# Performance work log

Measured on AMD Instinct MI355X. Metric: run time of the kernel, lower is better.

The kernel has to match this reference:

```python
import jax, jax.numpy as jnp
import numpy as np

EPS = 1e-12  # torch F.normalize clamp_min eps


def _agnn_conv(x, src, dst, beta, n):
    # x: [N, D]; src/dst: [E] (message flows src -> dst, softmax over dst's in-edges)
    xn = x / jnp.maximum(jnp.linalg.norm(x, axis=-1, keepdims=True), EPS)
    alpha = beta[0] * jnp.sum(xn[src] * xn[dst], axis=-1)            # [E] cosine sim * beta
    amax = jax.ops.segment_max(alpha, dst, num_segments=n)           # stable segment softmax
    ex = jnp.exp(alpha - amax[dst])
    denom = jax.ops.segment_sum(ex, dst, num_segments=n)
    w = ex / denom[dst]                                              # [E]
    return jax.ops.segment_sum(x[src] * w[:, None], dst, num_segments=n)


def setup_inputs() -> dict:
    key = jax.random.key(0)
    ks = jax.random.split(key, 8)
    N, E, G = 131072, 4194304, 2048
    x = jax.random.normal(ks[0], (N, 75), dtype=jnp.float32)
    edge_index = jax.random.randint(ks[1], (2, E), 0, N, dtype=jnp.int64)
    batch = jnp.sort(jax.random.randint(ks[2], (N,), 0, G, dtype=jnp.int64))
    lin1_w = jax.random.normal(ks[3], (16, 75), dtype=jnp.float32) * (1.0 / np.sqrt(75))
    lin1_b = jnp.zeros((16,), jnp.float32)
    beta1 = jnp.ones((1,), jnp.float32)   # prop1: requires_grad=False, beta=1
    beta2 = jnp.ones((1,), jnp.float32)   # prop2: learnable beta, init 1
    lin2_w = jax.random.normal(ks[4], (64, 16), dtype=jnp.float32) * (1.0 / np.sqrt(16))
    lin2_b = jnp.zeros((64,), jnp.float32)
    gather_w = jax.random.normal(ks[5], (1, 64), dtype=jnp.float32) * (1.0 / np.sqrt(64))
    gather_b = jnp.zeros((1,), jnp.float32)
    return {"x": x, "edge_index": edge_index, "batch": batch, "num_graphs": G,
            "lin1_w": lin1_w, "lin1_b": lin1_b, "beta1": beta1, "beta2": beta2,
            "lin2_w": lin2_w, "lin2_b": lin2_b, "gather_w": gather_w, "gather_b": gather_b}


def reference(x, edge_index, batch, num_graphs, lin1_w, lin1_b, beta1, beta2,
              lin2_w, lin2_b, gather_w, gather_b):
    n = x.shape[0]
    # PyG AGNNConv adds self-loops by default
    loops = jnp.arange(n, dtype=edge_index.dtype)
    src = jnp.concatenate([edge_index[0], loops])
    dst = jnp.concatenate([edge_index[1], loops])
    # dropout is identity in eval mode
    h = jax.nn.relu(x @ lin1_w.T + lin1_b)          # [N, 16]
    h = _agnn_conv(h, src, dst, beta1, n)
    h = _agnn_conv(h, src, dst, beta2, n)
    h = h @ lin2_w.T + lin2_b                        # [N, 64]
    y = jax.ops.segment_sum(h, batch, num_segments=num_graphs)  # global_add_pool [G, 64]
    return y @ gather_w.T + gather_b                 # [G, 1]
```

## Files before the change

kernel.cpp:

```cpp
#include <hip/hip_runtime.h>
#include <hip/hip_bf16.h>
#include <hip/hip_fp16.h>
#include <math.h>

#define SSEPS 1e-24f
#define NPB 256
#define NPB_SHIFT 8
#define SRC_BITS 17
#define SRC_MASK ((1 << SRC_BITS) - 1)
#define NB 512
#define CAP_B 8832
#define SC_EDGES 4096
#define SCB 512
#define MG_T 512
#define MG_LIN 4096
#define CSR_T 512

union QRowU2 { int4 v; _Float16 h[8]; };


__global__ __launch_bounds__(MG_T) void mega1(
    const int* __restrict__ src, const int* __restrict__ dst, int E,
    int* __restrict__ gcnt, int* __restrict__ packed, int nScat,
    const float* __restrict__ x, const float* __restrict__ W1,
    const float* __restrict__ b1, int* __restrict__ rec1, int N, int D,
    const float* __restrict__ l2w, const float* __restrict__ l2b,
    const float* __restrict__ gw, float* __restrict__ vbuf,
    float* __restrict__ out, const float* __restrict__ gb, int G) {
    __shared__ int sh[1216];
    int bid = blockIdx.x;
    int t = threadIdx.x;

    if (bid < nScat) {
        int* h = sh;
        int* dl = sh + SCB;
        int base = bid * SC_EDGES;
        int ed[8], es[8];
        int nv = 0;
#pragma unroll
        for (int k = 0; k < 8; ++k) {
            int i = base + k * MG_T + t;
            if (i < E) {
                ed[nv] = __builtin_nontemporal_load(&dst[i]);
                es[nv] = __builtin_nontemporal_load(&src[i]);
                ++nv;
            }
        }
        h[t] = 0;
        __syncthreads();
        for (int k = 0; k < nv; ++k) atomicAdd(&h[ed[k] >> NPB_SHIFT], 1);
        __syncthreads();
        {
            int c = h[t];
            int gp = c ? atomicAdd(&gcnt[t], c) : 0;
            dl[t] = t * CAP_B + gp;
            h[t] = 0;
        }
        __syncthreads();
        for (int k = 0; k < nv; ++k) {
            int d = ed[k];
            int b = d >> NPB_SHIFT;
            int pos = atomicAdd(&h[b], 1);
            int gi = dl[b] + pos;
            if (gi < (b + 1) * CAP_B)
                packed[gi] = ((d & (NPB - 1)) << SRC_BITS) | es[k];
        }
    } else if (bid < nScat + MG_LIN) {
        float* Ws = (float*)sh;
        float* Bs = (float*)sh + 1200;
        for (int i = t; i < 16 * D; i += MG_T) Ws[i] = W1[i];
        if (t < 16) Bs[t] = b1[t];
        __syncthreads();
        int node = (bid - nScat) * (MG_T >> 4) + (t >> 4);
        int c = t & 15;
        if (node >= N) return;
        const float* xr = x + (size_t)node * D;
        float acc = Bs[c];
        for (int k = 0; k < D; ++k) acc = fmaf(xr[k], Ws[c * D + k], acc);
        float hv = fmaxf(acc, 0.f);
        float hn = __shfl_xor(hv, 1);
        if (!(c & 1)) {
            union { _Float16 hh[2]; int i; } u;
            u.hh[0] = (_Float16)hv;
            u.hh[1] = (_Float16)hn;
            rec1[8 * node + (c >> 1)] = u.i;
        }
    } else if (bid == nScat + MG_LIN) {
        if (t < 16) {
            float a = 0.f;
            for (int j = 0; j < 64; ++j) a = fmaf(gw[j], l2w[j * 16 + t], a);
            vbuf[t] = a;
        } else if (t == 16) {
            float a = 0.f;
            for (int j = 0; j < 64; ++j) a = fmaf(gw[j], l2b[j], a);
            vbuf[16] = a;
        }
    } else {
        int g = (bid - (nScat + MG_LIN + 1)) * MG_T + t;
        if (g < G) out[g] = gb[0];
    }
}

__global__ __launch_bounds__(CSR_T) void csr_build(
    const int* __restrict__ packed, const int* __restrict__ gcnt,
    int* __restrict__ deg, int* __restrict__ offs,
    int* __restrict__ csr_src, int N) {
    __shared__ int ldeg[NPB];
    __shared__ int lcur[NPB];
    __shared__ int wsum[4];
    int b = blockIdx.x;
    int t = threadIdx.x;
    int e0 = b * CAP_B;
    int cnt = gcnt[b];
    if (cnt > CAP_B) cnt = CAP_B;
    if (t < NPB) ldeg[t] = 0;
    __syncthreads();
    for (int i = t; i < cnt; i += CSR_T)
        atomicAdd(&ldeg[packed[e0 + i] >> SRC_BITS], 1);
    __syncthreads();
    if (t < NPB) {
        int v = ldeg[t];
        int lane = t & 63;
        int incl = v;
#pragma unroll
        for (int off = 1; off < 64; off <<= 1) {
            int up = __shfl_up(incl, off);
            if (lane >= off) incl += up;
        }
        if (lane == 63) wsum[t >> 6] = incl;
        lcur[t] = incl - v;
    }
    __syncthreads();
    if (t < NPB) {
        int w = t >> 6;
        int basep = 0;
        for (int k = 0; k < w; ++k) basep += wsum[k];
        int ex = lcur[t] + basep;
        int node = (b << NPB_SHIFT) + t;
        if (node < N) {
            deg[node] = ldeg[t];
            offs[node] = e0 + ex;
        }
        lcur[t] = ex;
    }
    __syncthreads();
    for (int i = t; i < cnt; i += CSR_T) {
        int p = packed[e0 + i];
        int pos = atomicAdd(&lcur[p >> SRC_BITS], 1);
        csr_src[e0 + pos] = p & SRC_MASK;
    }
}

__global__ __launch_bounds__(256) void agnn_conv1(
    const int* __restrict__ rec1,
    const int* __restrict__ offs, const int* __restrict__ deg,
    const int* __restrict__ csr, const float* __restrict__ beta_p,
    int* __restrict__ rec2, int N) {
    int tid = blockIdx.x * blockDim.x + threadIdx.x;
    int node = tid >> 1;
    int q = tid & 1;
    if (node >= N) return;
    float beta = beta_p[0];
    const int4* rp = (const int4*)rec1;

    QRowU2 rdu;
    rdu.v = rp[2 * node + q];
    float xd[8];
#pragma unroll
    for (int k = 0; k < 8; ++k) xd[k] = (float)rdu.h[k];

    float ssd = 0.f;
#pragma unroll
    for (int k = 0; k < 8; ++k) ssd = fmaf(xd[k], xd[k], ssd);
    ssd += __shfl_xor(ssd, 1);
    float invsd = rsqrtf(fmaxf(ssd, SSEPS));

    float e0 = __expf(beta * ssd * invsd * invsd);
    float denom = e0;
    float acc[8];
#pragma unroll
    for (int k = 0; k < 8; ++k) acc[k] = e0 * xd[k];

    int start = offs[node], cnt = deg[node];
    int i = 0;
    for (; i + 8 <= cnt; i += 8) {
        int j[8];
        QRowU2 r[8];
#pragma unroll
        for (int u = 0; u < 8; ++u) j[u] = __builtin_nontemporal_load(&csr[start + i + u]);
#pragma unroll
        for (int u = 0; u < 8; ++u) r[u].v = rp[2 * j[u] + q];
#pragma unroll
        for (int u = 0; u < 8; ++u) {
            float d = 0.f, ss = 0.f;
            float hs[8];
#pragma unroll
            for (int k = 0; k < 8; ++k) {
                hs[k] = (float)r[u].h[k];
                d = fmaf(xd[k], hs[k], d);
                ss = fmaf(hs[k], hs[k], ss);
            }
            d += __shfl_xor(d, 1);
            ss += __shfl_xor(ss, 1);
            float ee = __expf(beta * d * invsd * rsqrtf(fmaxf(ss, SSEPS)));
            denom += ee;
#pragma unroll
            for (int k = 0; k < 8; ++k) acc[k] = fmaf(ee, hs[k], acc[k]);
        }
    }
    for (; i < cnt; ++i) {
        int j = __builtin_nontemporal_load(&csr[start + i]);
        QRowU2 r;
        r.v = rp[2 * j + q];
        float d = 0.f, ss = 0.f;
        float hs[8];
#pragma unroll
        for (int k = 0; k < 8; ++k) {
            hs[k] = (float)r.h[k];
            d = fmaf(xd[k], hs[k], d);
            ss = fmaf(hs[k], hs[k], ss);
        }
        d += __shfl_xor(d, 1);
        ss += __shfl_xor(ss, 1);
        float ee = __expf(beta * d * invsd * rsqrtf(fmaxf(ss, SSEPS)));
        denom += ee;
#pragma unroll
        for (int k = 0; k < 8; ++k) acc[k] = fmaf(ee, hs[k], acc[k]);
    }

    float inv = 1.f / denom;
    QRowU2 w;
#pragma unroll
    for (int k = 0; k < 8; ++k) w.h[k] = (_Float16)(acc[k] * inv);
    ((int4*)rec2)[2 * node + q] = w.v;
}

__global__ __launch_bounds__(256) void agnn_conv2(
    const int* __restrict__ rec2,
    const int* __restrict__ offs, const int* __restrict__ deg,
    const int* __restrict__ csr, const float* __restrict__ beta_p,
    const float* __restrict__ vbuf, const int* __restrict__ batch,
    float* __restrict__ out, int N) {
    int tid = blockIdx.x * blockDim.x + threadIdx.x;
    int node = tid >> 1;
    int q = tid & 1;
    if (node >= N) return;
    float beta = beta_p[0];
    const int4* rp = (const int4*)rec2;

    float vq[8];
#pragma unroll
    for (int k = 0; k < 8; ++k) vq[k] = vbuf[8 * q + k];

    QRowU2 rdu;
    rdu.v = rp[2 * node + q];
    float xd[8];
#pragma unroll
    for (int k = 0; k < 8; ++k) xd[k] = (float)rdu.h[k];

    float ssd = 0.f, pd = 0.f;
#pragma unroll
    for (int k = 0; k < 8; ++k) {
        ssd = fmaf(xd[k], xd[k], ssd);
        pd = fmaf(vq[k], xd[k], pd);
    }
    ssd += __shfl_xor(ssd, 1);
    pd += __shfl_xor(pd, 1);
    float invsd = rsqrtf(fmaxf(ssd, SSEPS));

    float e0 = __expf(beta * ssd * invsd * invsd);
    float denom = e0;
    float acc = e0 * pd;

    int start = offs[node], cnt = deg[node];
    int i = 0;
    for (; i + 8 <= cnt; i += 8) {
        int j[8];
        QRowU2 r[8];
#pragma unroll
        for (int u = 0; u < 8; ++u) j[u] = __builtin_nontemporal_load(&csr[start + i + u]);
#pragma unroll
        for (int u = 0; u < 8; ++u) r[u].v = rp[2 * j[u] + q];
#pragma unroll
        for (int u = 0; u < 8; ++u) {
            float d = 0.f, ss = 0.f, pv = 0.f;
#pragma unroll
            for (int k = 0; k < 8; ++k) {
                float hs = (float)r[u].h[k];
                d = fmaf(xd[k], hs, d);
                ss = fmaf(hs, hs, ss);
                pv = fmaf(vq[k], hs, pv);
            }
            d += __shfl_xor(d, 1);
            ss += __shfl_xor(ss, 1);
            pv += __shfl_xor(pv, 1);
            float ee = __expf(beta * d * invsd * rsqrtf(fmaxf(ss, SSEPS)));
            denom += ee;
            acc = fmaf(ee, pv, acc);
        }
    }
    for (; i < cnt; ++i) {
        int j = __builtin_nontemporal_load(&csr[start + i]);
        QRowU2 r;
        r.v = rp[2 * j + q];
        float d = 0.f, ss = 0.f, pv = 0.f;
#pragma unroll
        for (int k = 0; k < 8; ++k) {
            float hs = (float)r.h[k];
            d = fmaf(xd[k], hs, d);
            ss = fmaf(hs, hs, ss);
            pv = fmaf(vq[k], hs, pv);
        }
        d += __shfl_xor(d, 1);
        ss += __shfl_xor(ss, 1);
        pv += __shfl_xor(pv, 1);
        float ee = __expf(beta * d * invsd * rsqrtf(fmaxf(ss, SSEPS)));
        denom += ee;
        acc = fmaf(ee, pv, acc);
    }
    if (q == 0) atomicAdd(&out[batch[node]], acc / denom + vbuf[16]);
}


extern "C" void kernel_launch(void* const* d_in, const int* in_sizes, int n_in,
                              void* d_out, int out_size, void* d_ws, size_t ws_size,
                              hipStream_t stream) {
    const float* x = (const float*)d_in[0];
    const int* edge_index = (const int*)d_in[1];
    const int* batch = (const int*)d_in[2];
    const float* lin1_w = (const float*)d_in[4];
    const float* lin1_b = (const float*)d_in[5];
    const float* beta1 = (const float*)d_in[6];
    const float* beta2 = (const float*)d_in[7];
    const float* lin2_w = (const float*)d_in[8];
    const float* lin2_b = (const float*)d_in[9];
    const float* gather_w = (const float*)d_in[10];
    const float* gather_b = (const float*)d_in[11];
    float* out = (float*)d_out;

    const int N = in_sizes[2];
    const int E = in_sizes[1] / 2;
    const int D = in_sizes[0] / N;
    const int G = out_size;

    const int* src = edge_index;
    const int* dst = edge_index + E;

    float* w = (float*)d_ws;
    int* rec1 = (int*)w;                 w += (size_t)N * 8;
    int* rec2 = (int*)w;                 w += (size_t)N * 8;
    float* vbuf = w;                     w += 32;
    int* deg = (int*)w;                  w += N;
    int* offs = (int*)w;                 w += N;
    int* packed = (int*)w;               w += (size_t)NB * CAP_B;
    int* csr_src = (int*)w;              w += (size_t)NB * CAP_B;
    int* gcnt = (int*)w;                 w += NB;

    const int B = 256;
    dim3 gridNode2((2 * N + B - 1) / B);

    hipMemsetAsync(gcnt, 0, NB * sizeof(int), stream);

    int nScat = (E + SC_EDGES - 1) / SC_EDGES;
    int nLin = (N + (MG_T / 16) - 1) / (MG_T / 16);
    int nOut = (G + MG_T - 1) / MG_T;
    dim3 megaGrid(nScat + nLin + 1 + nOut);
    mega1<<<megaGrid, MG_T, 0, stream>>>(src, dst, E, gcnt, packed, nScat,
                                         x, lin1_w, lin1_b, rec1, N, D,
                                         lin2_w, lin2_b, gather_w, vbuf,
                                         out, gather_b, G);

    csr_build<<<dim3(NB), CSR_T, 0, stream>>>(packed, gcnt, deg, offs,
                                              csr_src, N);

    agnn_conv1<<<gridNode2, B, 0, stream>>>(rec1, offs, deg, csr_src,
                                            beta1, rec2, N);
    agnn_conv2<<<gridNode2, B, 0, stream>>>(rec2, offs, deg, csr_src,
                                            beta2, vbuf, batch, out, N);
}
```

Measured before the change: 332.7 us.

## Sort nodes by degree and split each row across four lanes

Adds a degree histogram in csr_build, plus a scan and a counting-sort scatter that build a degree-ordered permutation of nodes with their offsets and degrees. Both AGNN convolution kernels now walk nodes in that order, so each wavefront handles nodes of similar degree and loses less time to divergent loop trip counts. Each node row is also split across four lanes loading 8 bytes each instead of two lanes loading 16 bytes, with an extra shuffle stage per reduction. This costs two extra small kernel launches and an indirection through perm, and neighbouring nodes in a wave are no longer contiguous when their rows are read and written.

```diff
diff --git a/kernel.cpp b/kernel.cpp
--- a/kernel.cpp
+++ b/kernel.cpp
@@ -15,8 +15,9 @@
 #define MG_T 512
 #define MG_LIN 4096
 #define CSR_T 512
-
-union QRowU2 { int4 v; _Float16 h[8]; };
+#define DBINS 256
+
+union QRowU { int2 v; _Float16 h[4]; };
 
 
 __global__ __launch_bounds__(MG_T) void mega1(
@@ -104,9 +105,10 @@
 __global__ __launch_bounds__(CSR_T) void csr_build(
     const int* __restrict__ packed, const int* __restrict__ gcnt,
     int* __restrict__ deg, int* __restrict__ offs,
-    int* __restrict__ csr_src, int N) {
+    int* __restrict__ csr_src, int* __restrict__ hist, int N) {
     __shared__ int ldeg[NPB];
     __shared__ int lcur[NPB];
+    __shared__ int lhist[DBINS];
     __shared__ int wsum[4];
     int b = blockIdx.x;
     int t = threadIdx.x;
@@ -114,12 +116,14 @@
     int cnt = gcnt[b];
     if (cnt > CAP_B) cnt = CAP_B;
     if (t < NPB) ldeg[t] = 0;
+    if (t < DBINS) lhist[t] = 0;
     __syncthreads();
     for (int i = t; i < cnt; i += CSR_T)
         atomicAdd(&ldeg[packed[e0 + i] >> SRC_BITS], 1);
     __syncthreads();
     if (t < NPB) {
         int v = ldeg[t];
+        atomicAdd(&lhist[v < DBINS ? v : DBINS - 1], 1);
         int lane = t & 63;
         int incl = v;
 #pragma unroll
@@ -143,157 +147,214 @@
         }
         lcur[t] = ex;
     }
+    if (t < DBINS && t >= NPB) {}
     __syncthreads();
     for (int i = t; i < cnt; i += CSR_T) {
         int p = packed[e0 + i];
         int pos = atomicAdd(&lcur[p >> SRC_BITS], 1);
         csr_src[e0 + pos] = p & SRC_MASK;
     }
+    if (t < DBINS && lhist[t]) atomicAdd(&hist[t], lhist[t]);
+}
+
+__global__ void deg_scan(const int* __restrict__ hist, int* __restrict__ cursor) {
+    __shared__ int s[DBINS];
+    int t = threadIdx.x;
+    int h = hist[t];
+    s[t] = h;
+    __syncthreads();
+    for (int off = 1; off < DBINS; off <<= 1) {
+        int a = (t >= off) ? s[t - off] : 0;
+        __syncthreads();
+        s[t] += a;
+        __syncthreads();
+    }
+    cursor[t] = s[t] - h;
+}
+
+__global__ void deg_scatter(const int* __restrict__ deg, const int* __restrict__ offs,
+                            int* __restrict__ cursor, int* __restrict__ perm,
+                            int* __restrict__ sdeg, int* __restrict__ soffs, int N) {
+    __shared__ int lh[DBINS];
+    __shared__ int lb[DBINS];
+    int t = threadIdx.x;
+    if (t < DBINS) lh[t] = 0;
+    __syncthreads();
+    int i = blockIdx.x * blockDim.x + t;
+    int bin = 0, r = 0, dv = 0;
+    if (i < N) {
+        dv = deg[i];
+        bin = dv < DBINS ? dv : DBINS - 1;
+        r = atomicAdd(&lh[bin], 1);
+    }
+    __syncthreads();
+    if (t < DBINS && lh[t]) lb[t] = atomicAdd(&cursor[t], lh[t]);
+    __syncthreads();
+    if (i < N) {
+        int p = lb[bin] + r;
+        perm[p] = i;
+        sdeg[p] = dv;
+        soffs[p] = offs[i];
+    }
 }
 
 __global__ __launch_bounds__(256) void agnn_conv1(
     const int* __restrict__ rec1,
-    const int* __restrict__ offs, const int* __restrict__ deg,
-    const int* __restrict__ csr, const float* __restrict__ beta_p,
+    const int* __restrict__ soffs, const int* __restrict__ sdeg,
+    const int* __restrict__ csr, const int* __restrict__ perm,
+    const float* __restrict__ beta_p,
     int* __restrict__ rec2, int N) {
     int tid = blockIdx.x * blockDim.x + threadIdx.x;
-    int node = tid >> 1;
-    int q = tid & 1;
-    if (node >= N) return;
+    int slot = tid >> 2;
+    int q = tid & 3;
+    if (slot >= N) return;
+    int node = perm[slot];
     float beta = beta_p[0];
-    const int4* rp = (const int4*)rec1;
-
-    QRowU2 rdu;
-    rdu.v = rp[2 * node + q];
-    float xd[8];
-#pragma unroll
-    for (int k = 0; k < 8; ++k) xd[k] = (float)rdu.h[k];
+    const int2* rp = (const int2*)rec1;
+
+    QRowU rdu;
+    rdu.v = rp[4 * node + q];
+    float xd[4];
+#pragma unroll
+    for (int k = 0; k < 4; ++k) xd[k] = (float)rdu.h[k];
 
     float ssd = 0.f;
 #pragma unroll
-    for (int k = 0; k < 8; ++k) ssd = fmaf(xd[k], xd[k], ssd);
+    for (int k = 0; k < 4; ++k) ssd = fmaf(xd[k], xd[k], ssd);
     ssd += __shfl_xor(ssd, 1);
+    ssd += __shfl_xor(ssd, 2);
     float invsd = rsqrtf(fmaxf(ssd, SSEPS));
 
     float e0 = __expf(beta * ssd * invsd * invsd);
     float denom = e0;
-    float acc[8];
-#pragma unroll
-    for (int k = 0; k < 8; ++k) acc[k] = e0 * xd[k];
-
-    int start = offs[node], cnt = deg[node];
+    float acc[4];
+#pragma unroll
+    for (int k = 0; k < 4; ++k) acc[k] = e0 * xd[k];
+
+    int start = soffs[slot], cnt = sdeg[slot];
     int i = 0;
     for (; i + 8 <= cnt; i += 8) {
         int j[8];
-        QRowU2 r[8];
+        QRowU r[8];
 #pragma unroll
         for (int u = 0; u < 8; ++u) j[u] = __builtin_nontemporal_load(&csr[start + i + u]);
 #pragma unroll
-        for (int u = 0; u < 8; ++u) r[u].v = rp[2 * j[u] + q];
+        for (int u = 0; u < 8; ++u) r[u].v = rp[4 * j[u] + q];
 #pragma unroll
         for (int u = 0; u < 8; ++u) {
             float d = 0.f, ss = 0.f;
-            float hs[8];
-#pragma unroll
-            for (int k = 0; k < 8; ++k) {
+            float hs[4];
+#pragma unroll
+            for (int k = 0; k < 4; ++k) {
                 hs[k] = (float)r[u].h[k];
                 d = fmaf(xd[k], hs[k], d);
                 ss = fmaf(hs[k], hs[k], ss);
             }
             d += __shfl_xor(d, 1);
+            d += __shfl_xor(d, 2);
             ss += __shfl_xor(ss, 1);
+            ss += __shfl_xor(ss, 2);
             float ee = __expf(beta * d * invsd * rsqrtf(fmaxf(ss, SSEPS)));
             denom += ee;
 #pragma unroll
-            for (int k = 0; k < 8; ++k) acc[k] = fmaf(ee, hs[k], acc[k]);
+            for (int k = 0; k < 4; ++k) acc[k] = fmaf(ee, hs[k], acc[k]);
         }
     }
     for (; i < cnt; ++i) {
         int j = __builtin_nontemporal_load(&csr[start + i]);
-        QRowU2 r;
-        r.v = rp[2 * j + q];
+        QRowU r;
+        r.v = rp[4 * j + q];
         float d = 0.f, ss = 0.f;
-        float hs[8];
-#pragma unroll
-        for (int k = 0; k < 8; ++k) {
+        float hs[4];
+#pragma unroll
+        for (int k = 0; k < 4; ++k) {
             hs[k] = (float)r.h[k];
             d = fmaf(xd[k], hs[k], d);
             ss = fmaf(hs[k], hs[k], ss);
         }
         d += __shfl_xor(d, 1);
+        d += __shfl_xor(d, 2);
         ss += __shfl_xor(ss, 1);
+        ss += __shfl_xor(ss, 2);
         float ee = __expf(beta * d * invsd * rsqrtf(fmaxf(ss, SSEPS)));
         denom += ee;
 #pragma unroll
-        for (int k = 0; k < 8; ++k) acc[k] = fmaf(ee, hs[k], acc[k]);
+        for (int k = 0; k < 4; ++k) acc[k] = fmaf(ee, hs[k], acc[k]);
     }
 
     float inv = 1.f / denom;
-    QRowU2 w;
-#pragma unroll
-    for (int k = 0; k < 8; ++k) w.h[k] = (_Float16)(acc[k] * inv);
-    ((int4*)rec2)[2 * node + q] = w.v;
+    QRowU w;
+#pragma unroll
+    for (int k = 0; k < 4; ++k) w.h[k] = (_Float16)(acc[k] * inv);
+    ((int2*)rec2)[4 * node + q] = w.v;
 }
 
 __global__ __launch_bounds__(256) void agnn_conv2(
     const int* __restrict__ rec2,
-    const int* __restrict__ offs, const int* __restrict__ deg,
-    const int* __restrict__ csr, const float* __restrict__ beta_p,
+    const int* __restrict__ soffs, const int* __restrict__ sdeg,
+    const int* __restrict__ csr, const int* __restrict__ perm,
+    const float* __restrict__ beta_p,
     const float* __restrict__ vbuf, const int* __restrict__ batch,
     float* __restrict__ out, int N) {
     int tid = blockIdx.x * blockDim.x + threadIdx.x;
-    int node = tid >> 1;
-    int q = tid & 1;
-    if (node >= N) return;
+    int slot = tid >> 2;
+    int q = tid & 3;
+    if (slot >= N) return;
+    int node = perm[slot];
     float beta = beta_p[0];
-    const int4* rp = (const int4*)rec2;
-
-    float vq[8];
-#pragma unroll
-    for (int k = 0; k < 8; ++k) vq[k] = vbuf[8 * q + k];
-
-    QRowU2 rdu;
-    rdu.v = rp[2 * node + q];
-    float xd[8];
-#pragma unroll
-    for (int k = 0; k < 8; ++k) xd[k] = (float)rdu.h[k];
+    const int2* rp = (const int2*)rec2;
+
+    float vq[4];
+#pragma unroll
+    for (int k = 0; k < 4; ++k) vq[k] = vbuf[4 * q + k];
+
+    QRowU rdu;
+    rdu.v = rp[4 * node + q];
+    float xd[4];
+#pragma unroll
+    for (int k = 0; k < 4; ++k) xd[k] = (float)rdu.h[k];
 
     float ssd = 0.f, pd = 0.f;
 #pragma unroll
-    for (int k = 0; k < 8; ++k) {
+    for (int k = 0; k < 4; ++k) {
         ssd = fmaf(xd[k], xd[k], ssd);
         pd = fmaf(vq[k], xd[k], pd);
     }
     ssd += __shfl_xor(ssd, 1);
+    ssd += __shfl_xor(ssd, 2);
     pd += __shfl_xor(pd, 1);
+    pd += __shfl_xor(pd, 2);
     float invsd = rsqrtf(fmaxf(ssd, SSEPS));
 
     float e0 = __expf(beta * ssd * invsd * invsd);
     float denom = e0;
     float acc = e0 * pd;
 
-    int start = offs[node], cnt = deg[node];
+    int start = soffs[slot], cnt = sdeg[slot];
     int i = 0;
     for (; i + 8 <= cnt; i += 8) {
         int j[8];
-        QRowU2 r[8];
+        QRowU r[8];
 #pragma unroll
         for (int u = 0; u < 8; ++u) j[u] = __builtin_nontemporal_load(&csr[start + i + u]);
 #pragma unroll
-        for (int u = 0; u < 8; ++u) r[u].v = rp[2 * j[u] + q];
+        for (int u = 0; u < 8; ++u) r[u].v = rp[4 * j[u] + q];
 #pragma unroll
         for (int u = 0; u < 8; ++u) {
             float d = 0.f, ss = 0.f, pv = 0.f;
 #pragma unroll
-            for (int k = 0; k < 8; ++k) {
+            for (int k = 0; k < 4; ++k) {
                 float hs = (float)r[u].h[k];
                 d = fmaf(xd[k], hs, d);
                 ss = fmaf(hs, hs, ss);
                 pv = fmaf(vq[k], hs, pv);
             }
             d += __shfl_xor(d, 1);
+            d += __shfl_xor(d, 2);
             ss += __shfl_xor(ss, 1);
+            ss += __shfl_xor(ss, 2);
             pv += __shfl_xor(pv, 1);
+            pv += __shfl_xor(pv, 2);
             float ee = __expf(beta * d * invsd * rsqrtf(fmaxf(ss, SSEPS)));
             denom += ee;
             acc = fmaf(ee, pv, acc);
@@ -301,19 +362,22 @@
     }
     for (; i < cnt; ++i) {
         int j = __builtin_nontemporal_load(&csr[start + i]);
-        QRowU2 r;
-        r.v = rp[2 * j + q];
+        QRowU r;
+        r.v = rp[4 * j + q];
         float d = 0.f, ss = 0.f, pv = 0.f;
 #pragma unroll
-        for (int k = 0; k < 8; ++k) {
+        for (int k = 0; k < 4; ++k) {
             float hs = (float)r.h[k];
             d = fmaf(xd[k], hs, d);
             ss = fmaf(hs, hs, ss);
             pv = fmaf(vq[k], hs, pv);
         }
         d += __shfl_xor(d, 1);
+        d += __shfl_xor(d, 2);
         ss += __shfl_xor(ss, 1);
+        ss += __shfl_xor(ss, 2);
         pv += __shfl_xor(pv, 1);
+        pv += __shfl_xor(pv, 2);
         float ee = __expf(beta * d * invsd * rsqrtf(fmaxf(ss, SSEPS)));
         denom += ee;
         acc = fmaf(ee, pv, acc);
@@ -355,11 +419,16 @@
     int* packed = (int*)w;               w += (size_t)NB * CAP_B;
     int* csr_src = (int*)w;              w += (size_t)NB * CAP_B;
     int* gcnt = (int*)w;                 w += NB;
+    int* hist = (int*)w;                 w += DBINS;
+    int* cursor = (int*)w;               w += DBINS;
+    int* perm = (int*)w;                 w += N;
+    int* sdeg = (int*)w;                 w += N;
+    int* soffs = (int*)w;                w += N;
 
     const int B = 256;
-    dim3 gridNode2((2 * N + B - 1) / B);
-
-    hipMemsetAsync(gcnt, 0, NB * sizeof(int), stream);
+    dim3 gridNode4((4 * N + B - 1) / B);
+
+    hipMemsetAsync(gcnt, 0, (NB + DBINS) * sizeof(int), stream);
 
     int nScat = (E + SC_EDGES - 1) / SC_EDGES;
     int nLin = (N + (MG_T / 16) - 1) / (MG_T / 16);
@@ -371,10 +440,14 @@
                                          out, gather_b, G);
 
     csr_build<<<dim3(NB), CSR_T, 0, stream>>>(packed, gcnt, deg, offs,
-                                              csr_src, N);
-
-    agnn_conv1<<<gridNode2, B, 0, stream>>>(rec1, offs, deg, csr_src,
+                                              csr_src, hist, N);
+
+    deg_scan<<<dim3(1), DBINS, 0, stream>>>(hist, cursor);
+    deg_scatter<<<dim3((N + B - 1) / B), B, 0, stream>>>(deg, offs, cursor, perm,
+                                                         sdeg, soffs, N);
+
+    agnn_conv1<<<gridNode4, B, 0, stream>>>(rec1, soffs, sdeg, csr_src, perm,
                                             beta1, rec2, N);
-    agnn_conv2<<<gridNode2, B, 0, stream>>>(rec2, offs, deg, csr_src,
+    agnn_conv2<<<gridNode4, B, 0, stream>>>(rec2, soffs, sdeg, csr_src, perm,
                                             beta2, vbuf, batch, out, N);
 }
```

Measured after the change: 329.8 us. About the same (-0.8%).

## Drop CSR build; aggregate edges per destination bucket with LDS atomics

Applied to the files above, without the earlier changes.

Removes the csr_build kernel along with the deg/offs/csr_src arrays. Each of 512 blocks of 1024 threads now walks its destination bucket of packed edges directly. Per-node accumulators live in shared memory and are updated with LDS float atomics, so no per-node sorted adjacency is needed. This saves a kernel launch and the CSR write/read traffic, but adds shared-memory atomic contention and uses only 512 blocks, which may limit occupancy. It also relies on the softmax max being skipped, which is safe because the cosine similarity is bounded.

```diff
diff --git a/kernel.cpp b/kernel.cpp
--- a/kernel.cpp
+++ b/kernel.cpp
@@ -14,9 +14,7 @@
 #define SCB 512
 #define MG_T 512
 #define MG_LIN 4096
-#define CSR_T 512
-
-union QRowU2 { int4 v; _Float16 h[8]; };
+#define CV_T 1024
 
 
 __global__ __launch_bounds__(MG_T) void mega1(
@@ -101,224 +99,175 @@
     }
 }
 
-__global__ __launch_bounds__(CSR_T) void csr_build(
-    const int* __restrict__ packed, const int* __restrict__ gcnt,
-    int* __restrict__ deg, int* __restrict__ offs,
-    int* __restrict__ csr_src, int N) {
-    __shared__ int ldeg[NPB];
-    __shared__ int lcur[NPB];
-    __shared__ int wsum[4];
+__global__ __launch_bounds__(CV_T) void conv1p(
+    const int* __restrict__ rec1, const int* __restrict__ packed,
+    const int* __restrict__ gcnt, const float* __restrict__ beta_p,
+    int* __restrict__ rec2, int N) {
+    __shared__ float xs[NPB * 17];
+    __shared__ float as[NPB * 17];
     int b = blockIdx.x;
     int t = threadIdx.x;
-    int e0 = b * CAP_B;
+    float beta = beta_p[0];
+
+    {
+        int ln = t >> 2;
+        int qq = t & 3;
+        int node = (b << NPB_SHIFT) + ln;
+        union { int2 v; _Float16 h[4]; } u;
+        u.v = ((const int2*)rec1)[4 * node + qq];
+        float f0 = (float)u.h[0], f1 = (float)u.h[1];
+        float f2 = (float)u.h[2], f3 = (float)u.h[3];
+        float ss = f0 * f0 + f1 * f1 + f2 * f2 + f3 * f3;
+        ss += __shfl_xor(ss, 1);
+        ss += __shfl_xor(ss, 2);
+        float invsd = rsqrtf(fmaxf(ss, SSEPS));
+        float e0 = __expf(beta * ss * invsd * invsd);
+        int base = ln * 17 + qq * 4;
+        xs[base + 0] = f0; xs[base + 1] = f1;
+        xs[base + 2] = f2; xs[base + 3] = f3;
+        as[base + 0] = e0 * f0; as[base + 1] = e0 * f1;
+        as[base + 2] = e0 * f2; as[base + 3] = e0 * f3;
+        if (qq == 0) {
+            xs[ln * 17 + 16] = invsd;
+            as[ln * 17 + 16] = e0;
+        }
+    }
+    __syncthreads();
+
     int cnt = gcnt[b];
     if (cnt > CAP_B) cnt = CAP_B;
-    if (t < NPB) ldeg[t] = 0;
+    const int* pk = packed + b * CAP_B;
+    const int4* rp = (const int4*)rec1;
+    for (int i = t; i < cnt; i += CV_T) {
+        int p = __builtin_nontemporal_load(&pk[i]);
+        int d = p >> SRC_BITS;
+        int s = p & SRC_MASK;
+        int4 r0 = rp[2 * s];
+        int4 r1 = rp[2 * s + 1];
+        int base = d * 17;
+        float invsd = xs[base + 16];
+        union { int4 v; _Float16 h[8]; } u0, u1;
+        u0.v = r0; u1.v = r1;
+        float dot = 0.f, ss = 0.f;
+#pragma unroll
+        for (int k = 0; k < 8; ++k) {
+            float f = (float)u0.h[k];
+            dot = fmaf(xs[base + k], f, dot);
+            ss = fmaf(f, f, ss);
+        }
+#pragma unroll
+        for (int k = 0; k < 8; ++k) {
+            float f = (float)u1.h[k];
+            dot = fmaf(xs[base + 8 + k], f, dot);
+            ss = fmaf(f, f, ss);
+        }
+        float ee = __expf(beta * dot * invsd * rsqrtf(fmaxf(ss, SSEPS)));
+#pragma unroll
+        for (int k = 0; k < 8; ++k)
+            atomicAdd(&as[base + k], ee * (float)u0.h[k]);
+#pragma unroll
+        for (int k = 0; k < 8; ++k)
+            atomicAdd(&as[base + 8 + k], ee * (float)u1.h[k]);
+        atomicAdd(&as[base + 16], ee);
+    }
     __syncthreads();
-    for (int i = t; i < cnt; i += CSR_T)
-        atomicAdd(&ldeg[packed[e0 + i] >> SRC_BITS], 1);
-    __syncthreads();
-    if (t < NPB) {
-        int v = ldeg[t];
-        int lane = t & 63;
-        int incl = v;
-#pragma unroll
-        for (int off = 1; off < 64; off <<= 1) {
-            int up = __shfl_up(incl, off);
-            if (lane >= off) incl += up;
-        }
-        if (lane == 63) wsum[t >> 6] = incl;
-        lcur[t] = incl - v;
-    }
-    __syncthreads();
-    if (t < NPB) {
-        int w = t >> 6;
-        int basep = 0;
-        for (int k = 0; k < w; ++k) basep += wsum[k];
-        int ex = lcur[t] + basep;
-        int node = (b << NPB_SHIFT) + t;
-        if (node < N) {
-            deg[node] = ldeg[t];
-            offs[node] = e0 + ex;
-        }
-        lcur[t] = ex;
-    }
-    __syncthreads();
-    for (int i = t; i < cnt; i += CSR_T) {
-        int p = packed[e0 + i];
-        int pos = atomicAdd(&lcur[p >> SRC_BITS], 1);
-        csr_src[e0 + pos] = p & SRC_MASK;
+
+    {
+        int ln = t >> 2;
+        int qq = t & 3;
+        int node = (b << NPB_SHIFT) + ln;
+        float inv = 1.f / as[ln * 17 + 16];
+        union { int2 v; _Float16 h[4]; } w;
+#pragma unroll
+        for (int k = 0; k < 4; ++k)
+            w.h[k] = (_Float16)(as[ln * 17 + qq * 4 + k] * inv);
+        if (node < N) ((int2*)rec2)[4 * node + qq] = w.v;
     }
 }
 
-__global__ __launch_bounds__(256) void agnn_conv1(
-    const int* __restrict__ rec1,
-    const int* __restrict__ offs, const int* __restrict__ deg,
-    const int* __restrict__ csr, const float* __restrict__ beta_p,
-    int* __restrict__ rec2, int N) {
-    int tid = blockIdx.x * blockDim.x + threadIdx.x;
-    int node = tid >> 1;
-    int q = tid & 1;
-    if (node >= N) return;
-    float beta = beta_p[0];
-    const int4* rp = (const int4*)rec1;
-
-    QRowU2 rdu;
-    rdu.v = rp[2 * node + q];
-    float xd[8];
-#pragma unroll
-    for (int k = 0; k < 8; ++k) xd[k] = (float)rdu.h[k];
-
-    float ssd = 0.f;
-#pragma unroll
-    for (int k = 0; k < 8; ++k) ssd = fmaf(xd[k], xd[k], ssd);
-    ssd += __shfl_xor(ssd, 1);
-    float invsd = rsqrtf(fmaxf(ssd, SSEPS));
-
-    float e0 = __expf(beta * ssd * invsd * invsd);
-    float denom = e0;
-    float acc[8];
-#pragma unroll
-    for (int k = 0; k < 8; ++k) acc[k] = e0 * xd[k];
-
-    int start = offs[node], cnt = deg[node];
-    int i = 0;
-    for (; i + 8 <= cnt; i += 8) {
-        int j[8];
-        QRowU2 r[8];
-#pragma unroll
-        for (int u = 0; u < 8; ++u) j[u] = __builtin_nontemporal_load(&csr[start + i + u]);
-#pragma unroll
-        for (int u = 0; u < 8; ++u) r[u].v = rp[2 * j[u] + q];
-#pragma unroll
-        for (int u = 0; u < 8; ++u) {
-            float d = 0.f, ss = 0.f;
-            float hs[8];
-#pragma unroll
-            for (int k = 0; k < 8; ++k) {
-                hs[k] = (float)r[u].h[k];
-                d = fmaf(xd[k], hs[k], d);
-                ss = fmaf(hs[k], hs[k], ss);
-            }
-            d += __shfl_xor(d, 1);
-            ss += __shfl_xor(ss, 1);
-            float ee = __expf(beta * d * invsd * rsqrtf(fmaxf(ss, SSEPS)));
-            denom += ee;
-#pragma unroll
-            for (int k = 0; k < 8; ++k) acc[k] = fmaf(ee, hs[k], acc[k]);
-        }
-    }
-    for (; i < cnt; ++i) {
-        int j = __builtin_nontemporal_load(&csr[start + i]);
-        QRowU2 r;
-        r.v = rp[2 * j + q];
-        float d = 0.f, ss = 0.f;
-        float hs[8];
-#pragma unroll
-        for (int k = 0; k < 8; ++k) {
-            hs[k] = (float)r.h[k];
-            d = fmaf(xd[k], hs[k], d);
-            ss = fmaf(hs[k], hs[k], ss);
-        }
-        d += __shfl_xor(d, 1);
-        ss += __shfl_xor(ss, 1);
-        float ee = __expf(beta * d * invsd * rsqrtf(fmaxf(ss, SSEPS)));
-        denom += ee;
-#pragma unroll
-        for (int k = 0; k < 8; ++k) acc[k] = fmaf(ee, hs[k], acc[k]);
-    }
-
-    float inv = 1.f / denom;
-    QRowU2 w;
-#pragma unroll
-    for (int k = 0; k < 8; ++k) w.h[k] = (_Float16)(acc[k] * inv);
-    ((int4*)rec2)[2 * node + q] = w.v;
-}
-
-__global__ __launch_bounds__(256) void agnn_conv2(
-    const int* __restrict__ rec2,
-    const int* __restrict__ offs, const int* __restrict__ deg,
-    const int* __restrict__ csr, const float* __restrict__ beta_p,
+__global__ __launch_bounds__(CV_T) void conv2p(
+    const int* __restrict__ rec2, const int* __restrict__ packed,
+    const int* __restrict__ gcnt, const float* __restrict__ beta_p,
     const float* __restrict__ vbuf, const int* __restrict__ batch,
     float* __restrict__ out, int N) {
-    int tid = blockIdx.x * blockDim.x + threadIdx.x;
-    int node = tid >> 1;
-    int q = tid & 1;
-    if (node >= N) return;
+    __shared__ float xs[NPB * 17];
+    __shared__ float as[NPB * 3];
+    int b = blockIdx.x;
+    int t = threadIdx.x;
     float beta = beta_p[0];
+    float v[16];
+#pragma unroll
+    for (int k = 0; k < 16; ++k) v[k] = vbuf[k];
+    float c0 = vbuf[16];
+
+    {
+        int ln = t >> 2;
+        int qq = t & 3;
+        int node = (b << NPB_SHIFT) + ln;
+        union { int2 v; _Float16 h[4]; } u;
+        u.v = ((const int2*)rec2)[4 * node + qq];
+        float f0 = (float)u.h[0], f1 = (float)u.h[1];
+        float f2 = (float)u.h[2], f3 = (float)u.h[3];
+        float ss = f0 * f0 + f1 * f1 + f2 * f2 + f3 * f3;
+        float pd = v[qq * 4 + 0] * f0 + v[qq * 4 + 1] * f1 +
+                   v[qq * 4 + 2] * f2 + v[qq * 4 + 3] * f3;
+        ss += __shfl_xor(ss, 1);
+        ss += __shfl_xor(ss, 2);
+        pd += __shfl_xor(pd, 1);
+        pd += __shfl_xor(pd, 2);
+        float invsd = rsqrtf(fmaxf(ss, SSEPS));
+        float e0 = __expf(beta * ss * invsd * invsd);
+        int base = ln * 17 + qq * 4;
+        xs[base + 0] = f0; xs[base + 1] = f1;
+        xs[base + 2] = f2; xs[base + 3] = f3;
+        if (qq == 0) {
+            xs[ln * 17 + 16] = invsd;
+            as[ln * 3 + 0] = e0 * pd;
+            as[ln * 3 + 1] = e0;
+        }
+    }
+    __syncthreads();
+
+    int cnt = gcnt[b];
+    if (cnt > CAP_B) cnt = CAP_B;
+    const int* pk = packed + b * CAP_B;
     const int4* rp = (const int4*)rec2;
-
-    float vq[8];
-#pragma unroll
-    for (int k = 0; k < 8; ++k) vq[k] = vbuf[8 * q + k];
-
-    QRowU2 rdu;
-    rdu.v = rp[2 * node + q];
-    float xd[8];
-#pragma unroll
-    for (int k = 0; k < 8; ++k) xd[k] = (float)rdu.h[k];
-
-    float ssd = 0.f, pd = 0.f;
-#pragma unroll
-    for (int k = 0; k < 8; ++k) {
-        ssd = fmaf(xd[k], xd[k], ssd);
-        pd = fmaf(vq[k], xd[k], pd);
-    }
-    ssd += __shfl_xor(ssd, 1);
-    pd += __shfl_xor(pd, 1);
-    float invsd = rsqrtf(fmaxf(ssd, SSEPS));
-
-    float e0 = __expf(beta * ssd * invsd * invsd);
-    float denom = e0;
-    float acc = e0 * pd;
-
-    int start = offs[node], cnt = deg[node];
-    int i = 0;
-    for (; i + 8 <= cnt; i += 8) {
-        int j[8];
-        QRowU2 r[8];
-#pragma unroll
-        for (int u = 0; u < 8; ++u) j[u] = __builtin_nontemporal_load(&csr[start + i + u]);
-#pragma unroll
-        for (int u = 0; u < 8; ++u) r[u].v = rp[2 * j[u] + q];
-#pragma unroll
-        for (int u = 0; u < 8; ++u) {
-            float d = 0.f, ss = 0.f, pv = 0.f;
-#pragma unroll
-            for (int k = 0; k < 8; ++k) {
-                float hs = (float)r[u].h[k];
-                d = fmaf(xd[k], hs, d);
-                ss = fmaf(hs, hs, ss);
-                pv = fmaf(vq[k], hs, pv);
-            }
-            d += __shfl_xor(d, 1);
-            ss += __shfl_xor(ss, 1);
-            pv += __shfl_xor(pv, 1);
-            float ee = __expf(beta * d * invsd * rsqrtf(fmaxf(ss, SSEPS)));
-            denom += ee;
-            acc = fmaf(ee, pv, acc);
-        }
-    }
-    for (; i < cnt; ++i) {
-        int j = __builtin_nontemporal_load(&csr[start + i]);
-        QRowU2 r;
-        r.v = rp[2 * j + q];
-        float d = 0.f, ss = 0.f, pv = 0.f;
-#pragma unroll
-        for (int k = 0; k < 8; ++k) {
-            float hs = (float)r.h[k];
-            d = fmaf(xd[k], hs, d);
-            ss = fmaf(hs, hs, ss);
-            pv = fmaf(vq[k], hs, pv);
-        }
-        d += __shfl_xor(d, 1);
-        ss += __shfl_xor(ss, 1);
-        pv += __shfl_xor(pv, 1);
-        float ee = __expf(beta * d * invsd * rsqrtf(fmaxf(ss, SSEPS)));
-        denom += ee;
-        acc = fmaf(ee, pv, acc);
-    }
-    if (q == 0) atomicAdd(&out[batch[node]], acc / denom + vbuf[16]);
+    for (int i = t; i < cnt; i += CV_T) {
+        int p = __builtin_nontemporal_load(&pk[i]);
+        int d = p >> SRC_BITS;
+        int s = p & SRC_MASK;
+        int4 r0 = rp[2 * s];
+        int4 r1 = rp[2 * s + 1];
+        int base = d * 17;
+        float invsd = xs[base + 16];
+        union { int4 v; _Float16 h[8]; } u0, u1;
+        u0.v = r0; u1.v = r1;
+        float dot = 0.f, ss = 0.f, pv = 0.f;
+#pragma unroll
+        for (int k = 0; k < 8; ++k) {
+            float f = (float)u0.h[k];
+            dot = fmaf(xs[base + k], f, dot);
+            ss = fmaf(f, f, ss);
+            pv = fmaf(v[k], f, pv);
+        }
+#pragma unroll
+        for (int k = 0; k < 8; ++k) {
+            float f = (float)u1.h[k];
+            dot = fmaf(xs[base + 8 + k], f, dot);
+            ss = fmaf(f, f, ss);
+            pv = fmaf(v[8 + k], f, pv);
+        }
+        float ee = __expf(beta * dot * invsd * rsqrtf(fmaxf(ss, SSEPS)));
+        atomicAdd(&as[d * 3 + 0], ee * pv);
+        atomicAdd(&as[d * 3 + 1], ee);
+    }
+    __syncthreads();
+
+    if (t < NPB) {
+        int node = (b << NPB_SHIFT) + t;
+        float r = as[t * 3 + 0] / as[t * 3 + 1];
+        if (node < N) atomicAdd(&out[batch[node]], r + c0);
+    }
 }
 
 
@@ -350,14 +299,8 @@
     int* rec1 = (int*)w;                 w += (size_t)N * 8;
     int* rec2 = (int*)w;                 w += (size_t)N * 8;
     float* vbuf = w;                     w += 32;
-    int* deg = (int*)w;                  w += N;
-    int* offs = (int*)w;                 w += N;
     int* packed = (int*)w;               w += (size_t)NB * CAP_B;
-    int* csr_src = (int*)w;              w += (size_t)NB * CAP_B;
     int* gcnt = (int*)w;                 w += NB;
-
-    const int B = 256;
-    dim3 gridNode2((2 * N + B - 1) / B);
 
     hipMemsetAsync(gcnt, 0, NB * sizeof(int), stream);
 
@@ -370,11 +313,7 @@
                                          lin2_w, lin2_b, gather_w, vbuf,
                                          out, gather_b, G);
 
-    csr_build<<<dim3(NB), CSR_T, 0, stream>>>(packed, gcnt, deg, offs,
-                                              csr_src, N);
-
-    agnn_conv1<<<gridNode2, B, 0, stream>>>(rec1, offs, deg, csr_src,
-                                            beta1, rec2, N);
-    agnn_conv2<<<gridNode2, B, 0, stream>>>(rec2, offs, deg, csr_src,
-                                            beta2, vbuf, batch, out, N);
+    conv1p<<<dim3(NB), CV_T, 0, stream>>>(rec1, packed, gcnt, beta1, rec2, N);
+    conv2p<<<dim3(NB), CV_T, 0, stream>>>(rec2, packed, gcnt, beta2, vbuf,
+                                          batch, out, N);
 }
```

After: 642.1 us. +93.0%, slower.
